# Kernel tuning notes

Measured on AMD Instinct MI355X. Metric: run time of the kernel, lower is better.

Reference implementation:

```python
import jax, jax.numpy as jnp
import numpy as np

SI = 4   # input window size
SO = 2   # output sub-grid per window


def _compute_padding(dim, stride):
    if dim % stride == 0:
        return (0, 0)
    pad = (dim // stride + 1) * stride - dim
    return (pad // 2, pad - pad // 2)


def setup_inputs() -> dict:
    key = jax.random.key(0)
    k1, k2, k3 = jax.random.split(key, 3)
    x = jax.random.normal(k1, (16, 256, 128, 128), dtype=jnp.float32)
    w_key = jax.random.normal(k2, (64, 256), dtype=jnp.float32) * 0.05   # conv1x1 dim->key_dim
    w_sim = jax.random.normal(k3, (4, 64), dtype=jnp.float32) * 0.05     # conv1x1 key_dim->so^2
    return {"x": x, "w_key": w_key, "w_sim": w_sim}


def reference(x, w_key, w_sim):
    si, so = SI, SO
    N, C, H, W = x.shape
    pad_t, pad_b = _compute_padding(H, si)
    pad_l, pad_r = _compute_padding(W, si)
    x = jnp.pad(x, ((0, 0), (0, 0), (pad_t, pad_b), (pad_l, pad_r)))
    N, C, H, W = x.shape
    h, w = H // si, W // si
    so2, si2 = so * so, si * si

    # 1x1 convs: key = relu(Wk x), kq = Ws key
    key = jax.nn.relu(jnp.einsum('nchw,kc->nkhw', x, w_key))
    kq = jnp.einsum('nkhw,sk->nshw', key, w_sim)              # [N, so^2, H, W]

    # windowize: [N, C, h, w, si*si] -> [N, h, w, C, si*si]
    xw = x.reshape(N, C, h, si, w, si).transpose(0, 2, 4, 1, 3, 5).reshape(N, h, w, C, si2)
    # kq windows: [N, h, w, si*si, so^2]
    kqw = kq.reshape(N, so2, h, si, w, si).transpose(0, 2, 4, 3, 5, 1).reshape(N, h, w, si2, so2)
    kqw = jax.nn.softmax(kqw / si, axis=3)

    # per-window softmax-weighted aggregation: [N,h,w,C,so^2]
    out = jnp.einsum('nhwcp,nhwpq->nhwcq', xw, kqw)
    out = out.reshape(N, h, w, C, so, so).transpose(0, 3, 1, 4, 2, 5)
    return out.reshape(N, C, h * so, w * so)
```

## Files before the change

### kernel.cpp

```cpp
#include <hip/hip_runtime.h>
#include <cstdint>


#define CIN 256

typedef __attribute__((ext_vector_type(8))) short short8;
typedef __attribute__((ext_vector_type(4))) float floatx4;

__device__ __forceinline__ short f2bf_rn(float f) {
    union { float f; uint32_t u; } v; v.f = f;
    uint32_t u = v.u + 0x7fffu + ((v.u >> 16) & 1u);
    return (short)(u >> 16);
}
__device__ __forceinline__ short f2bf_rh(float f) {
    union { float f; uint32_t u; } v; v.f = f;
    return (short)((v.u + 0x8000u) >> 16);
}

__global__ void cvt_wkey_kernel(const float* __restrict__ wk,
                                short* __restrict__ wkb) {
    int i = blockIdx.x * 256 + threadIdx.x;
    wkb[i] = f2bf_rn(wk[i]);
}

__global__ __launch_bounds__(256, 8) void fds_kernel(
    const float* __restrict__ x, const short* __restrict__ wkb,
    const float* __restrict__ wsim, float* __restrict__ out)
{
    __shared__ short xs[16][264];
    __shared__ float keyS[16][68];
    __shared__ float partS[256];
    __shared__ float wgtS[64];

    const int b   = blockIdx.x;
    const int wid = (b & 7) * 2048 + (b >> 3);
    const int n   = wid >> 10;
    const int hh  = (wid >> 5) & 31;
    const int ww  = wid & 31;
    const int t   = threadIdx.x;

    float v[16];
    {
        const float* xb = x + (((size_t)(n * CIN + t) * 128 + hh * 4) * 128 + ww * 4);
        float4 r0 = *(const float4*)(xb);
        float4 r1 = *(const float4*)(xb + 128);
        float4 r2 = *(const float4*)(xb + 256);
        float4 r3 = *(const float4*)(xb + 384);
        v[0]=r0.x;  v[1]=r0.y;  v[2]=r0.z;  v[3]=r0.w;
        v[4]=r1.x;  v[5]=r1.y;  v[6]=r1.z;  v[7]=r1.w;
        v[8]=r2.x;  v[9]=r2.y;  v[10]=r2.z; v[11]=r2.w;
        v[12]=r3.x; v[13]=r3.y; v[14]=r3.z; v[15]=r3.w;
        #pragma unroll
        for (int p = 0; p < 16; ++p) xs[p][t] = f2bf_rh(v[p]);
    }
    __syncthreads();

    {
        const int l    = t & 63;
        const int wv   = t >> 6;
        const int mrow = l & 15;
        const int kq8  = (l >> 4) * 8;
        floatx4 acc = {0.f, 0.f, 0.f, 0.f};
        #pragma unroll
        for (int ks = 0; ks < 8; ++ks) {
            short8 af  = *(const short8*)(&xs[mrow][ks * 32 + kq8]);
            short8 bfr = *(const short8*)(wkb + ((wv * 16 + mrow) * 256 + ks * 32 + kq8));
            acc = __builtin_amdgcn_mfma_f32_16x16x32_bf16(af, bfr, acc, 0, 0, 0);
        }
        #pragma unroll
        for (int r = 0; r < 4; ++r)
            keyS[(l >> 4) * 4 + r][wv * 16 + mrow] = fmaxf(acc[r], 0.f);
    }
    __syncthreads();

    {
        const int p  = t >> 4;
        const int s  = (t >> 2) & 3;
        const int kk = t & 3;
        const float4* kp = (const float4*)&keyS[p][kk * 16];
        const float4* wp = (const float4*)(wsim + s * 64 + kk * 16);
        float acc = 0.f;
        #pragma unroll
        for (int j = 0; j < 4; ++j) {
            float4 kj = kp[j];
            float4 wj = wp[j];
            acc += kj.x * wj.x + kj.y * wj.y + kj.z * wj.z + kj.w * wj.w;
        }
        partS[t] = acc;
    }
    __syncthreads();

    if (t < 64) {
        const int p = t >> 2, s = t & 3;
        float4 pr = *(const float4*)&partS[p * 16 + s * 4];
        float logit = 0.25f * (pr.x + pr.y + pr.z + pr.w);
        float m = logit;
        #pragma unroll
        for (int msk = 4; msk < 64; msk <<= 1)
            m = fmaxf(m, __shfl_xor(m, msk, 64));
        float e = __expf(logit - m);
        float ssum = e;
        #pragma unroll
        for (int msk = 4; msk < 64; msk <<= 1)
            ssum += __shfl_xor(ssum, msk, 64);
        wgtS[t] = e / ssum;
    }
    __syncthreads();

    {
        float a0 = 0.f, a1 = 0.f, a2 = 0.f, a3 = 0.f;
        #pragma unroll
        for (int p = 0; p < 16; ++p) {
            float4 wq = *(const float4*)&wgtS[p * 4];
            a0 += v[p] * wq.x;
            a1 += v[p] * wq.y;
            a2 += v[p] * wq.z;
            a3 += v[p] * wq.w;
        }
        float* ob = out + (((size_t)(n * CIN + t) * 64 + hh * 2) * 64 + ww * 2);
        *(float2*)(ob)      = make_float2(a0, a1);
        *(float2*)(ob + 64) = make_float2(a2, a3);
    }
}

extern "C" void kernel_launch(void* const* d_in, const int* in_sizes, int n_in,
                              void* d_out, int out_size, void* d_ws, size_t ws_size,
                              hipStream_t stream) {
    const float* x    = (const float*)d_in[0];
    const float* wkey = (const float*)d_in[1];
    const float* wsim = (const float*)d_in[2];
    float* out = (float*)d_out;
    short* wkb = (short*)d_ws;

    cvt_wkey_kernel<<<64, 256, 0, stream>>>(wkey, wkb);
    fds_kernel<<<16384, 256, 0, stream>>>(x, wkb, wsim, out);
}
```

Before: 449.1 us.

## Process four adjacent windows per block with coalesced loads and reused weight fragments

```diff
diff --git a/kernel.cpp b/kernel.cpp
--- a/kernel.cpp
+++ b/kernel.cpp
@@ -2,8 +2,11 @@
 #include <cstdint>
 
 
-#define CIN 256
+#define CIN  256
+#define CPAD 264
+#define KPAD 68
 
+typedef __attribute__((ext_vector_type(4))) short short4v;
 typedef __attribute__((ext_vector_type(8))) short short8;
 typedef __attribute__((ext_vector_type(4))) float floatx4;
 
@@ -16,6 +19,10 @@
     union { float f; uint32_t u; } v; v.f = f;
     return (short)((v.u + 0x8000u) >> 16);
 }
+__device__ __forceinline__ float bf2f(short s) {
+    union { uint32_t u; float f; } v; v.u = ((uint32_t)(uint16_t)s) << 16;
+    return v.f;
+}
 
 __global__ void cvt_wkey_kernel(const float* __restrict__ wk,
                                 short* __restrict__ wkb) {
@@ -23,103 +30,125 @@
     wkb[i] = f2bf_rn(wk[i]);
 }
 
-__global__ __launch_bounds__(256, 8) void fds_kernel(
+__global__ __launch_bounds__(256, 3) void fds_kernel(
     const float* __restrict__ x, const short* __restrict__ wkb,
     const float* __restrict__ wsim, float* __restrict__ out)
 {
-    __shared__ short xs[16][264];
-    __shared__ float keyS[16][68];
-    __shared__ float partS[256];
-    __shared__ float wgtS[64];
+    __shared__ alignas(16) short xs[64][CPAD];
+    __shared__ alignas(16) float keyS[64][KPAD];
+    __shared__ float logitS[64][4];
+    __shared__ float wgtS[256];
+    __shared__ float wsimS[256];
 
     const int b   = blockIdx.x;
-    const int wid = (b & 7) * 2048 + (b >> 3);
-    const int n   = wid >> 10;
-    const int hh  = (wid >> 5) & 31;
-    const int ww  = wid & 31;
+    const int wid = (b & 7) * 512 + (b >> 3);
+    const int n   = wid >> 8;
+    const int hh  = (wid >> 3) & 31;
+    const int wq  = wid & 7;
     const int t   = threadIdx.x;
 
-    float v[16];
-    {
-        const float* xb = x + (((size_t)(n * CIN + t) * 128 + hh * 4) * 128 + ww * 4);
-        float4 r0 = *(const float4*)(xb);
-        float4 r1 = *(const float4*)(xb + 128);
-        float4 r2 = *(const float4*)(xb + 256);
-        float4 r3 = *(const float4*)(xb + 384);
-        v[0]=r0.x;  v[1]=r0.y;  v[2]=r0.z;  v[3]=r0.w;
-        v[4]=r1.x;  v[5]=r1.y;  v[6]=r1.z;  v[7]=r1.w;
-        v[8]=r2.x;  v[9]=r2.y;  v[10]=r2.z; v[11]=r2.w;
-        v[12]=r3.x; v[13]=r3.y; v[14]=r3.z; v[15]=r3.w;
-        #pragma unroll
-        for (int p = 0; p < 16; ++p) xs[p][t] = f2bf_rh(v[p]);
+    if (t < 64) *(float4*)&wsimS[t * 4] = *(const float4*)(wsim + t * 4);
+
+    #pragma unroll
+    for (int i = 0; i < 4; ++i) {
+        const int idx  = i * 256 + t;
+        const int colg = idx & 3, r = (idx >> 2) & 3, cg = idx >> 4;
+        const float* xb = x + ((size_t)(n * CIN + cg * 4) << 14)
+                            + (hh * 4 + r) * 128 + wq * 16 + colg * 4;
+        float4 v0 = *(const float4*)(xb);
+        float4 v1 = *(const float4*)(xb + 16384);
+        float4 v2 = *(const float4*)(xb + 32768);
+        float4 v3 = *(const float4*)(xb + 49152);
+        const int pxb = colg * 16 + r * 4;
+        short4v w0 = { f2bf_rh(v0.x), f2bf_rh(v1.x), f2bf_rh(v2.x), f2bf_rh(v3.x) };
+        short4v w1 = { f2bf_rh(v0.y), f2bf_rh(v1.y), f2bf_rh(v2.y), f2bf_rh(v3.y) };
+        short4v w2 = { f2bf_rh(v0.z), f2bf_rh(v1.z), f2bf_rh(v2.z), f2bf_rh(v3.z) };
+        short4v w3 = { f2bf_rh(v0.w), f2bf_rh(v1.w), f2bf_rh(v2.w), f2bf_rh(v3.w) };
+        *(short4v*)&xs[pxb + 0][cg * 4] = w0;
+        *(short4v*)&xs[pxb + 1][cg * 4] = w1;
+        *(short4v*)&xs[pxb + 2][cg * 4] = w2;
+        *(short4v*)&xs[pxb + 3][cg * 4] = w3;
     }
     __syncthreads();
 
     {
-        const int l    = t & 63;
-        const int wv   = t >> 6;
-        const int mrow = l & 15;
-        const int kq8  = (l >> 4) * 8;
-        floatx4 acc = {0.f, 0.f, 0.f, 0.f};
+        const int l = t & 63, wv = t >> 6;
+        const int kr = l & 15, kq8 = (l >> 4) * 8;
+        short8 bfr[8];
         #pragma unroll
-        for (int ks = 0; ks < 8; ++ks) {
-            short8 af  = *(const short8*)(&xs[mrow][ks * 32 + kq8]);
-            short8 bfr = *(const short8*)(wkb + ((wv * 16 + mrow) * 256 + ks * 32 + kq8));
-            acc = __builtin_amdgcn_mfma_f32_16x16x32_bf16(af, bfr, acc, 0, 0, 0);
+        for (int ks = 0; ks < 8; ++ks)
+            bfr[ks] = *(const short8*)(wkb + (wv * 16 + kr) * 256 + ks * 32 + kq8);
+        #pragma unroll
+        for (int mt = 0; mt < 4; ++mt) {
+            floatx4 acc = {0.f, 0.f, 0.f, 0.f};
+            #pragma unroll
+            for (int ks = 0; ks < 8; ++ks) {
+                short8 af = *(const short8*)(&xs[mt * 16 + kr][ks * 32 + kq8]);
+                acc = __builtin_amdgcn_mfma_f32_16x16x32_bf16(af, bfr[ks], acc, 0, 0, 0);
+            }
+            #pragma unroll
+            for (int rg = 0; rg < 4; ++rg)
+                keyS[mt * 16 + (l >> 4) * 4 + rg][wv * 16 + kr] = fmaxf(acc[rg], 0.f);
         }
-        #pragma unroll
-        for (int r = 0; r < 4; ++r)
-            keyS[(l >> 4) * 4 + r][wv * 16 + mrow] = fmaxf(acc[r], 0.f);
     }
     __syncthreads();
 
     {
-        const int p  = t >> 4;
-        const int s  = (t >> 2) & 3;
-        const int kk = t & 3;
-        const float4* kp = (const float4*)&keyS[p][kk * 16];
-        const float4* wp = (const float4*)(wsim + s * 64 + kk * 16);
+        const int px = t >> 2, s = t & 3;
         float acc = 0.f;
         #pragma unroll
-        for (int j = 0; j < 4; ++j) {
-            float4 kj = kp[j];
-            float4 wj = wp[j];
-            acc += kj.x * wj.x + kj.y * wj.y + kj.z * wj.z + kj.w * wj.w;
+        for (int kk = 0; kk < 16; ++kk) {
+            float4 kv = *(const float4*)&keyS[px][kk * 4];
+            float4 wv4 = *(const float4*)&wsimS[s * 64 + kk * 4];
+            acc += kv.x * wv4.x + kv.y * wv4.y + kv.z * wv4.z + kv.w * wv4.w;
         }
-        partS[t] = acc;
+        logitS[px][s] = acc * 0.25f;
     }
     __syncthreads();
 
-    if (t < 64) {
-        const int p = t >> 2, s = t & 3;
-        float4 pr = *(const float4*)&partS[p * 16 + s * 4];
-        float logit = 0.25f * (pr.x + pr.y + pr.z + pr.w);
-        float m = logit;
+    {
+        const int p = t & 15, win = t >> 6;
+        float lg = logitS[win * 16 + p][(t >> 4) & 3];
+        float m = lg;
         #pragma unroll
-        for (int msk = 4; msk < 64; msk <<= 1)
+        for (int msk = 1; msk < 16; msk <<= 1)
             m = fmaxf(m, __shfl_xor(m, msk, 64));
-        float e = __expf(logit - m);
+        float e = __expf(lg - m);
         float ssum = e;
         #pragma unroll
-        for (int msk = 4; msk < 64; msk <<= 1)
+        for (int msk = 1; msk < 16; msk <<= 1)
             ssum += __shfl_xor(ssum, msk, 64);
         wgtS[t] = e / ssum;
     }
     __syncthreads();
 
     {
-        float a0 = 0.f, a1 = 0.f, a2 = 0.f, a3 = 0.f;
+        const int oc = t & 7, orr = (t >> 3) & 1, cgrp = t >> 4;
+        const int win = oc >> 1, q = orr * 2 + (oc & 1);
+        float wg[16];
+        #pragma unroll
+        for (int pk = 0; pk < 4; ++pk)
+            *(float4*)&wg[pk * 4] = *(const float4*)&wgtS[win * 64 + q * 16 + pk * 4];
+        float acc[16];
+        #pragma unroll
+        for (int i = 0; i < 16; ++i) acc[i] = 0.f;
         #pragma unroll
         for (int p = 0; p < 16; ++p) {
-            float4 wq = *(const float4*)&wgtS[p * 4];
-            a0 += v[p] * wq.x;
-            a1 += v[p] * wq.y;
-            a2 += v[p] * wq.z;
-            a3 += v[p] * wq.w;
+            const short* row = &xs[win * 16 + p][cgrp * 16];
+            short8 xa = *(const short8*)(row);
+            short8 xb2 = *(const short8*)(row + 8);
+            const float w = wg[p];
+            #pragma unroll
+            for (int j = 0; j < 8; ++j) {
+                acc[j]     += bf2f(xa[j])  * w;
+                acc[8 + j] += bf2f(xb2[j]) * w;
+            }
         }
-        float* ob = out + (((size_t)(n * CIN + t) * 64 + hh * 2) * 64 + ww * 2);
-        *(float2*)(ob)      = make_float2(a0, a1);
-        *(float2*)(ob + 64) = make_float2(a2, a3);
+        float* ob = out + ((size_t)(n * CIN + cgrp * 16) << 12)
+                        + (hh * 2 + orr) * 64 + wq * 8 + oc;
+        #pragma unroll
+        for (int i = 0; i < 16; ++i)
+            ob[(size_t)i << 12] = acc[i];
     }
 }
 
@@ -133,5 +162,5 @@
     short* wkb = (short*)d_ws;
 
     cvt_wkey_kernel<<<64, 256, 0, stream>>>(wkey, wkb);
-    fds_kernel<<<16384, 256, 0, stream>>>(x, wkb, wsim, out);
+    fds_kernel<<<4096, 256, 0, stream>>>(x, wkb, wsim, out);
 }
```

Measured after the change: 389.3 us. 13.3% less time.
